# Performance work log

Hardware: AMD Instinct MI355X
Metric: run time of the kernel (lower is better)

The kernel has to match this reference:

```python
import jax, jax.numpy as jnp
import numpy as np

N_HEAD = 8
D = 512
D_K = D // N_HEAD  # 64
B, S = 8, 1024


def setup_inputs() -> dict:
    key = jax.random.key(0)
    ks = jax.random.split(key, 7)
    scale = 1.0 / np.sqrt(D)  # ~ torch Linear init range
    return {
        "q": jax.random.normal(ks[0], (B, S, D), dtype=jnp.float32),
        "k": jax.random.normal(ks[1], (B, S, D), dtype=jnp.float32),
        "v": jax.random.normal(ks[2], (B, S, D), dtype=jnp.float32),
        # per-head Q/K projection weights, torch Linear convention W:[out,in]=[d_k,d]
        "Wq": jax.random.uniform(ks[3], (N_HEAD, D_K, D), jnp.float32, -scale, scale),
        "Wk": jax.random.uniform(ks[4], (N_HEAD, D_K, D), jnp.float32, -scale, scale),
        "Wv": jax.random.uniform(ks[5], (D_K, D), jnp.float32, -scale, scale),
        "Wo": jax.random.uniform(ks[6], (D, D_K), jnpp := jnp.float32, -1.0 / np.sqrt(D_K), 1.0 / np.sqrt(D_K)),
    }


def reference(q, k, v, Wq, Wk, Wv, Wo):
    # shared V projection: [B,S,d_k]
    vs = jnp.einsum("bsd,ed->bse", v, Wv)
    # batched per-head Q/K projections: [B,H,S,d_k]
    qh = jnp.einsum("bsd,hed->bhse", q, Wq)
    kh = jnp.einsum("bsd,hed->bhse", k, Wk)
    inv_sqrt_dk = 1.0 / jnp.sqrt(jnp.asarray(D_K, q.dtype))
    # scores [B,H,Sq,Sk], softmax over keys
    scores = jnp.einsum("bhqe,bhke->bhqk", qh * inv_sqrt_dk, kh)
    attn = jax.nn.softmax(scores, axis=-1)
    # shared V across heads, then mean over heads (interpretable combine)
    heads = jnp.einsum("bhqk,bke->bhqe", attn, vs)  # [B,H,S,d_k]
    head = heads.mean(axis=1)                        # [B,S,d_k]
    out = jnp.einsum("bse,de->bsd", head, Wo)        # [B,S,d]
    # torch.stack(attention) stacks over heads first -> [H,B,Sq,Sk]
    attn_stacked = jnp.transpose(attn, (1, 0, 2, 3))
    return out, attn_stacked
```

## Files before the change

kernel.cpp:

```cpp
#include <hip/hip_runtime.h>


using short8 = __attribute__((ext_vector_type(8))) short;
using f32x4  = __attribute__((ext_vector_type(4))) float;

static __device__ __forceinline__ short f2bf(float f) {
    union { float f; unsigned u; } x; x.f = f;
    unsigned r = x.u + 0x7fffu + ((x.u >> 16) & 1u);
    return (short)(r >> 16);
}
static __device__ __forceinline__ float bfhi2f(unsigned hi_bits) {
    union { unsigned u; float f; } x; x.u = hi_bits;
    return x.f;
}

__global__ __launch_bounds__(256) void gemm_proj(
    const float* __restrict__ A, const float* __restrict__ W,
    void* __restrict__ out, int M, int N, int K, float scale, int mode)
{
    __shared__ short As[128][40];
    __shared__ short Bs[128][40];

    const int tid  = threadIdx.x;
    const int m0   = blockIdx.x * 128;
    const int n0   = blockIdx.y * 128;
    const int lane = tid & 63, wave = tid >> 6;
    const int wm   = (wave & 1) * 64, wn = (wave >> 1) * 64;
    const int lrow = lane & 15, lq = lane >> 4;

    f32x4 acc[4][4] = {};

    for (int k0 = 0; k0 < K; k0 += 32) {
#pragma unroll
        for (int i = 0; i < 4; ++i) {
            int c = tid + i * 256;
            int row = c >> 3, c4 = c & 7;
            float4 v = *(const float4*)(A + (size_t)(m0 + row) * K + k0 + c4 * 4);
            short* dst = &As[row][c4 * 4];
            dst[0] = f2bf(v.x); dst[1] = f2bf(v.y); dst[2] = f2bf(v.z); dst[3] = f2bf(v.w);
        }
#pragma unroll
        for (int i = 0; i < 4; ++i) {
            int c = tid + i * 256;
            int row = c >> 3, c4 = c & 7;
            int gn = n0 + row;
            float4 v = make_float4(0.f, 0.f, 0.f, 0.f);
            if (gn < N) v = *(const float4*)(W + (size_t)gn * K + k0 + c4 * 4);
            short* dst = &Bs[row][c4 * 4];
            dst[0] = f2bf(v.x); dst[1] = f2bf(v.y); dst[2] = f2bf(v.z); dst[3] = f2bf(v.w);
        }
        __syncthreads();

        short8 af[4], bw[4];
#pragma unroll
        for (int i = 0; i < 4; ++i)
            af[i] = *(const short8*)&As[wm + i * 16 + lrow][lq * 8];
#pragma unroll
        for (int j = 0; j < 4; ++j)
            bw[j] = *(const short8*)&Bs[wn + j * 16 + lrow][lq * 8];
#pragma unroll
        for (int i = 0; i < 4; ++i)
#pragma unroll
            for (int j = 0; j < 4; ++j)
                acc[i][j] = __builtin_amdgcn_mfma_f32_16x16x32_bf16(af[i], bw[j], acc[i][j], 0, 0, 0);
        __syncthreads();
    }

#pragma unroll
    for (int i = 0; i < 4; ++i) {
#pragma unroll
        for (int j = 0; j < 4; ++j) {
#pragma unroll
            for (int r = 0; r < 4; ++r) {
                int m = m0 + wm + i * 16 + lq * 4 + r;
                int n = n0 + wn + j * 16 + lrow;
                if (n >= N) continue;
                float val = acc[i][j][r] * scale;
                if (mode == 0) {
                    int b = m >> 10, s = m & 1023;
                    int hh = n >> 6, e = n & 63;
                    ((short*)out)[(((size_t)(b * 8 + hh) * 1024 + s) << 6) + e] = f2bf(val);
                } else if (mode == 2) {
                    int b = m >> 10, s = m & 1023;
                    ((short*)out)[(((size_t)b * 64 + n) << 10) + s] = f2bf(val);
                } else {
                    ((float*)out)[(size_t)m * N + n] = val;
                }
            }
        }
    }
}

__global__ __launch_bounds__(256) void attn_fused(
    const short* __restrict__ qh,
    const short* __restrict__ kh,
    const short* __restrict__ vt,
    float* __restrict__ attn_out,
    float* __restrict__ head)
{
    __shared__ short qs[64][72];
    __shared__ short ks[128][72];
    __shared__ short vts[64][136];
    __shared__ short pa[4][16][136];

    const int bh = blockIdx.x;
    const int b = bh >> 3, h = bh & 7;
    const int qbase = blockIdx.y << 6;
    const int tid  = threadIdx.x;
    const int lane = tid & 63, wave = tid >> 6;
    const int lrow = lane & 15, lq = lane >> 4;

    const short* qp = qh + ((size_t)bh << 16);
    const short* kp = kh + ((size_t)bh << 16);
    const short* vp = vt + ((size_t)b << 16);

#pragma unroll
    for (int i = 0; i < 2; ++i) {
        int c = tid + i * 256;
        int row = c >> 3, c8 = c & 7;
        *(uint4*)&qs[row][c8 * 8] = *(const uint4*)(qp + (size_t)(qbase + row) * 64 + c8 * 8);
    }
    __syncthreads();

    short8 qf[2];
#pragma unroll
    for (int kk = 0; kk < 2; ++kk)
        qf[kk] = *(const short8*)&qs[wave * 16 + lrow][kk * 32 + lq * 8];

    float sume[4] = {0.f, 0.f, 0.f, 0.f};
    for (int kt = 0; kt < 1024; kt += 128) {
        __syncthreads();
#pragma unroll
        for (int i = 0; i < 4; ++i) {
            int c = tid + i * 256;
            int row = c >> 3, c8 = c & 7;
            *(uint4*)&ks[row][c8 * 8] = *(const uint4*)(kp + (size_t)(kt + row) * 64 + c8 * 8);
        }
        __syncthreads();
#pragma unroll
        for (int j = 0; j < 8; ++j) {
            f32x4 sc = {0.f, 0.f, 0.f, 0.f};
            short8 kb0 = *(const short8*)&ks[j * 16 + lrow][lq * 8];
            short8 kb1 = *(const short8*)&ks[j * 16 + lrow][32 + lq * 8];
            sc = __builtin_amdgcn_mfma_f32_16x16x32_bf16(qf[0], kb0, sc, 0, 0, 0);
            sc = __builtin_amdgcn_mfma_f32_16x16x32_bf16(qf[1], kb1, sc, 0, 0, 0);
#pragma unroll
            for (int r = 0; r < 4; ++r) sume[r] += __expf(sc[r]);
        }
    }
#pragma unroll
    for (int m = 1; m <= 8; m <<= 1)
#pragma unroll
        for (int r = 0; r < 4; ++r) sume[r] += __shfl_xor(sume[r], m, 64);
    float rinv[4];
#pragma unroll
    for (int r = 0; r < 4; ++r) rinv[r] = 1.0f / sume[r];

    f32x4 hacc[4] = {};
    for (int kt = 0; kt < 1024; kt += 128) {
        __syncthreads();
#pragma unroll
        for (int i = 0; i < 4; ++i) {
            int c = tid + i * 256;
            int row = c >> 3, c8 = c & 7;
            *(uint4*)&ks[row][c8 * 8] = *(const uint4*)(kp + (size_t)(kt + row) * 64 + c8 * 8);
        }
#pragma unroll
        for (int i = 0; i < 4; ++i) {
            int c = tid + i * 256;
            int row = c >> 4, c8 = c & 15;
            *(uint4*)&vts[row][c8 * 8] = *(const uint4*)(vp + ((size_t)row << 10) + kt + c8 * 8);
        }
        __syncthreads();

#pragma unroll
        for (int j = 0; j < 8; ++j) {
            f32x4 sc = {0.f, 0.f, 0.f, 0.f};
            short8 kb0 = *(const short8*)&ks[j * 16 + lrow][lq * 8];
            short8 kb1 = *(const short8*)&ks[j * 16 + lrow][32 + lq * 8];
            sc = __builtin_amdgcn_mfma_f32_16x16x32_bf16(qf[0], kb0, sc, 0, 0, 0);
            sc = __builtin_amdgcn_mfma_f32_16x16x32_bf16(qf[1], kb1, sc, 0, 0, 0);
#pragma unroll
            for (int r = 0; r < 4; ++r)
                pa[wave][lq * 4 + r][j * 16 + lrow] = f2bf(__expf(sc[r]) * rinv[r]);
        }

        size_t abase = (((size_t)(h * 8 + b) * 1024 + qbase + wave * 16) << 10) + kt;
#pragma unroll
        for (int i = 0; i < 4; ++i) {
            int c = lane + i * 64;
            int row = c >> 4, c8 = c & 15;
            uint4 pk = *(const uint4*)&pa[wave][row][c8 * 8];
            float4 v0, v1;
            v0.x = bfhi2f(pk.x << 16); v0.y = bfhi2f(pk.x & 0xffff0000u);
            v0.z = bfhi2f(pk.y << 16); v0.w = bfhi2f(pk.y & 0xffff0000u);
            v1.x = bfhi2f(pk.z << 16); v1.y = bfhi2f(pk.z & 0xffff0000u);
            v1.z = bfhi2f(pk.w << 16); v1.w = bfhi2f(pk.w & 0xffff0000u);
            float* gdst = attn_out + abase + ((size_t)row << 10) + c8 * 8;
            *(float4*)gdst       = v0;
            *(float4*)(gdst + 4) = v1;
        }

#pragma unroll
        for (int kk = 0; kk < 4; ++kk) {
            short8 af = *(const short8*)&pa[wave][lrow][kk * 32 + lq * 8];
#pragma unroll
            for (int cc = 0; cc < 4; ++cc) {
                short8 bv = *(const short8*)&vts[cc * 16 + lrow][kk * 32 + lq * 8];
                hacc[cc] = __builtin_amdgcn_mfma_f32_16x16x32_bf16(af, bv, hacc[cc], 0, 0, 0);
            }
        }
    }

#pragma unroll
    for (int cc = 0; cc < 4; ++cc)
#pragma unroll
        for (int r = 0; r < 4; ++r) {
            float v = hacc[cc][r] * 0.125f;
            atomicAdd(&head[(((size_t)b * 1024 + qbase + wave * 16 + lq * 4 + r) << 6) + cc * 16 + lrow], v);
        }
}

extern "C" void kernel_launch(void* const* d_in, const int* in_sizes, int n_in,
                              void* d_out, int out_size, void* d_ws, size_t ws_size,
                              hipStream_t stream)
{
    (void)in_sizes; (void)n_in; (void)out_size; (void)ws_size;

    const float* q  = (const float*)d_in[0];
    const float* k  = (const float*)d_in[1];
    const float* v  = (const float*)d_in[2];
    const float* Wq = (const float*)d_in[3];
    const float* Wk = (const float*)d_in[4];
    const float* Wv = (const float*)d_in[5];
    const float* Wo = (const float*)d_in[6];

    float* out  = (float*)d_out;
    float* attn = out + (size_t)8 * 1024 * 512;

    char* ws = (char*)d_ws;
    short* qh  = (short*)(ws);
    short* kh  = (short*)(ws + ((size_t)8  << 20));
    short* vt  = (short*)(ws + ((size_t)16 << 20));
    float* head = (float*)(ws + ((size_t)17 << 20));

    hipMemsetAsync(head, 0, (size_t)8 * 1024 * 64 * sizeof(float), stream);

    gemm_proj<<<dim3(64, 4), 256, 0, stream>>>(q, Wq, qh, 8192, 512, 512, 0.125f, 0);
    gemm_proj<<<dim3(64, 4), 256, 0, stream>>>(k, Wk, kh, 8192, 512, 512, 1.0f, 0);
    gemm_proj<<<dim3(64, 1), 256, 0, stream>>>(v, Wv, vt, 8192, 64, 512, 1.0f, 2);

    attn_fused<<<dim3(64, 16), 256, 0, stream>>>(qh, kh, vt, attn, head);

    gemm_proj<<<dim3(64, 4), 256, 0, stream>>>(head, Wo, out, 8192, 512, 64, 1.0f, 3);
}
```

Before: 517.4 us.

## Split attention into score and PV kernels, materializing exp scores

Splits the fused attention kernel into a scores kernel and a PV kernel. The scores kernel computes QK^T once, stores unnormalized bf16 exponentials and row reciprocal sums to workspace. The PV kernel reads them back, writes normalized attention, and does PV. This removes the recomputation of QK^T. Head outputs are now stored per head in bf16 and reduced by a K=512 output GEMM instead of atomics plus a memset. The V-projection epilogue is transposed through LDS for coalesced stores. In exchange it adds a large intermediate write and read through global memory.

```diff
diff --git a/kernel.cpp b/kernel.cpp
--- a/kernel.cpp
+++ b/kernel.cpp
@@ -16,10 +16,12 @@
 
 __global__ __launch_bounds__(256) void gemm_proj(
     const float* __restrict__ A, const float* __restrict__ W,
-    void* __restrict__ out, int M, int N, int K, float scale, int mode)
-{
-    __shared__ short As[128][40];
-    __shared__ short Bs[128][40];
+    short* __restrict__ out, int N, int K, float scale, int mode)
+{
+    __shared__ short smem[10240];
+    short (*As)[40] = (short(*)[40])smem;
+    short (*Bs)[40] = (short(*)[40])(smem + 5120);
+    short (*ts)[136] = (short(*)[136])smem;
 
     const int tid  = threadIdx.x;
     const int m0   = blockIdx.x * 128;
@@ -66,42 +68,132 @@
         __syncthreads();
     }
 
-#pragma unroll
-    for (int i = 0; i < 4; ++i) {
-#pragma unroll
-        for (int j = 0; j < 4; ++j) {
-#pragma unroll
-            for (int r = 0; r < 4; ++r) {
-                int m = m0 + wm + i * 16 + lq * 4 + r;
-                int n = n0 + wn + j * 16 + lrow;
-                if (n >= N) continue;
-                float val = acc[i][j][r] * scale;
-                if (mode == 0) {
+    if (mode == 0) {
+#pragma unroll
+        for (int i = 0; i < 4; ++i)
+#pragma unroll
+            for (int j = 0; j < 4; ++j)
+#pragma unroll
+                for (int r = 0; r < 4; ++r) {
+                    int m = m0 + wm + i * 16 + lq * 4 + r;
+                    int n = n0 + wn + j * 16 + lrow;
                     int b = m >> 10, s = m & 1023;
                     int hh = n >> 6, e = n & 63;
-                    ((short*)out)[(((size_t)(b * 8 + hh) * 1024 + s) << 6) + e] = f2bf(val);
-                } else if (mode == 2) {
-                    int b = m >> 10, s = m & 1023;
-                    ((short*)out)[(((size_t)b * 64 + n) << 10) + s] = f2bf(val);
-                } else {
-                    ((float*)out)[(size_t)m * N + n] = val;
+                    out[(((size_t)(b * 8 + hh) * 1024 + s) << 6) + e] =
+                        f2bf(acc[i][j][r] * scale);
                 }
-            }
-        }
-    }
-}
-
-__global__ __launch_bounds__(256) void attn_fused(
-    const short* __restrict__ qh,
-    const short* __restrict__ kh,
-    const short* __restrict__ vt,
-    float* __restrict__ attn_out,
-    float* __restrict__ head)
+    } else {
+        if (wn == 0) {
+#pragma unroll
+            for (int i = 0; i < 4; ++i)
+#pragma unroll
+                for (int j = 0; j < 4; ++j)
+#pragma unroll
+                    for (int r = 0; r < 4; ++r) {
+                        int ml = wm + i * 16 + lq * 4 + r;
+                        int n  = j * 16 + lrow;
+                        ts[n][ml] = f2bf(acc[i][j][r] * scale);
+                    }
+        }
+        __syncthreads();
+        int b = m0 >> 10, s0 = m0 & 1023;
+#pragma unroll
+        for (int i = 0; i < 4; ++i) {
+            int c = tid + i * 256;
+            int row = c >> 4, c16 = c & 15;
+            *(uint4*)(out + ((size_t)(b * 64 + row) << 10) + s0 + c16 * 8) =
+                *(const uint4*)&ts[row][c16 * 8];
+        }
+    }
+}
+
+__global__ __launch_bounds__(256) void attn_scores(
+    const short* __restrict__ qh, const short* __restrict__ kh,
+    short* __restrict__ expw, float* __restrict__ rinv)
 {
     __shared__ short qs[64][72];
     __shared__ short ks[128][72];
+    __shared__ short pa[64][136];
+
+    const int bh = blockIdx.x;
+    const int qbase = blockIdx.y << 6;
+    const int tid  = threadIdx.x;
+    const int lane = tid & 63, wave = tid >> 6;
+    const int lrow = lane & 15, lq = lane >> 4;
+
+    const short* qp = qh + ((size_t)bh << 16);
+    const short* kp = kh + ((size_t)bh << 16);
+    short* ep = expw + (((size_t)(bh << 10) + qbase) << 10);
+
+#pragma unroll
+    for (int i = 0; i < 2; ++i) {
+        int c = tid + i * 256;
+        int row = c >> 3, c8 = c & 7;
+        *(uint4*)&qs[row][c8 * 8] = *(const uint4*)(qp + (size_t)(qbase + row) * 64 + c8 * 8);
+    }
+    __syncthreads();
+
+    short8 qf[2];
+#pragma unroll
+    for (int kk = 0; kk < 2; ++kk)
+        qf[kk] = *(const short8*)&qs[wave * 16 + lrow][kk * 32 + lq * 8];
+
+    float sume[4] = {0.f, 0.f, 0.f, 0.f};
+
+    for (int kt = 0; kt < 1024; kt += 128) {
+        __syncthreads();
+#pragma unroll
+        for (int i = 0; i < 4; ++i) {
+            int c = tid + i * 256;
+            int row = c >> 3, c8 = c & 7;
+            *(uint4*)&ks[row][c8 * 8] = *(const uint4*)(kp + (size_t)(kt + row) * 64 + c8 * 8);
+        }
+        __syncthreads();
+
+#pragma unroll
+        for (int j = 0; j < 8; ++j) {
+            f32x4 sc = {0.f, 0.f, 0.f, 0.f};
+            short8 kb0 = *(const short8*)&ks[j * 16 + lrow][lq * 8];
+            short8 kb1 = *(const short8*)&ks[j * 16 + lrow][32 + lq * 8];
+            sc = __builtin_amdgcn_mfma_f32_16x16x32_bf16(qf[0], kb0, sc, 0, 0, 0);
+            sc = __builtin_amdgcn_mfma_f32_16x16x32_bf16(qf[1], kb1, sc, 0, 0, 0);
+#pragma unroll
+            for (int r = 0; r < 4; ++r) {
+                float e = __expf(sc[r]);
+                sume[r] += e;
+                pa[wave * 16 + lq * 4 + r][j * 16 + lrow] = f2bf(e);
+            }
+        }
+        __syncthreads();
+
+#pragma unroll
+        for (int i = 0; i < 4; ++i) {
+            int c = tid + i * 256;
+            int row = c >> 4, c16 = c & 15;
+            *(uint4*)(ep + ((size_t)row << 10) + kt + c16 * 8) =
+                *(const uint4*)&pa[row][c16 * 8];
+        }
+    }
+
+#pragma unroll
+    for (int m = 1; m <= 8; m <<= 1)
+#pragma unroll
+        for (int r = 0; r < 4; ++r) sume[r] += __shfl_xor(sume[r], m, 64);
+    if (lrow == 0) {
+#pragma unroll
+        for (int r = 0; r < 4; ++r)
+            rinv[(bh << 10) + qbase + wave * 16 + lq * 4 + r] = 1.0f / sume[r];
+    }
+}
+
+__global__ __launch_bounds__(256) void attn_pv(
+    const short* __restrict__ expw, const float* __restrict__ rinv,
+    const short* __restrict__ vt, float* __restrict__ attn_out,
+    short* __restrict__ headbf)
+{
+    __shared__ short es[64][136];
     __shared__ short vts[64][136];
-    __shared__ short pa[4][16][136];
+    __shared__ float rs[64];
 
     const int bh = blockIdx.x;
     const int b = bh >> 3, h = bh & 7;
@@ -110,100 +202,44 @@
     const int lane = tid & 63, wave = tid >> 6;
     const int lrow = lane & 15, lq = lane >> 4;
 
-    const short* qp = qh + ((size_t)bh << 16);
-    const short* kp = kh + ((size_t)bh << 16);
+    const short* ep = expw + (((size_t)(bh << 10) + qbase) << 10);
     const short* vp = vt + ((size_t)b << 16);
 
-#pragma unroll
-    for (int i = 0; i < 2; ++i) {
-        int c = tid + i * 256;
-        int row = c >> 3, c8 = c & 7;
-        *(uint4*)&qs[row][c8 * 8] = *(const uint4*)(qp + (size_t)(qbase + row) * 64 + c8 * 8);
-    }
-    __syncthreads();
-
-    short8 qf[2];
-#pragma unroll
-    for (int kk = 0; kk < 2; ++kk)
-        qf[kk] = *(const short8*)&qs[wave * 16 + lrow][kk * 32 + lq * 8];
-
-    float sume[4] = {0.f, 0.f, 0.f, 0.f};
+    if (tid < 64) rs[tid] = rinv[(bh << 10) + qbase + tid];
+
+    f32x4 hacc[4] = {};
+    const size_t abase0 = (((size_t)(h * 8 + b) * 1024 + qbase) << 10);
+
     for (int kt = 0; kt < 1024; kt += 128) {
         __syncthreads();
 #pragma unroll
         for (int i = 0; i < 4; ++i) {
             int c = tid + i * 256;
-            int row = c >> 3, c8 = c & 7;
-            *(uint4*)&ks[row][c8 * 8] = *(const uint4*)(kp + (size_t)(kt + row) * 64 + c8 * 8);
-        }
-        __syncthreads();
-#pragma unroll
-        for (int j = 0; j < 8; ++j) {
-            f32x4 sc = {0.f, 0.f, 0.f, 0.f};
-            short8 kb0 = *(const short8*)&ks[j * 16 + lrow][lq * 8];
-            short8 kb1 = *(const short8*)&ks[j * 16 + lrow][32 + lq * 8];
-            sc = __builtin_amdgcn_mfma_f32_16x16x32_bf16(qf[0], kb0, sc, 0, 0, 0);
-            sc = __builtin_amdgcn_mfma_f32_16x16x32_bf16(qf[1], kb1, sc, 0, 0, 0);
-#pragma unroll
-            for (int r = 0; r < 4; ++r) sume[r] += __expf(sc[r]);
-        }
-    }
-#pragma unroll
-    for (int m = 1; m <= 8; m <<= 1)
-#pragma unroll
-        for (int r = 0; r < 4; ++r) sume[r] += __shfl_xor(sume[r], m, 64);
-    float rinv[4];
-#pragma unroll
-    for (int r = 0; r < 4; ++r) rinv[r] = 1.0f / sume[r];
-
-    f32x4 hacc[4] = {};
-    for (int kt = 0; kt < 1024; kt += 128) {
-        __syncthreads();
-#pragma unroll
-        for (int i = 0; i < 4; ++i) {
-            int c = tid + i * 256;
-            int row = c >> 3, c8 = c & 7;
-            *(uint4*)&ks[row][c8 * 8] = *(const uint4*)(kp + (size_t)(kt + row) * 64 + c8 * 8);
-        }
-#pragma unroll
-        for (int i = 0; i < 4; ++i) {
-            int c = tid + i * 256;
-            int row = c >> 4, c8 = c & 15;
-            *(uint4*)&vts[row][c8 * 8] = *(const uint4*)(vp + ((size_t)row << 10) + kt + c8 * 8);
-        }
-        __syncthreads();
-
-#pragma unroll
-        for (int j = 0; j < 8; ++j) {
-            f32x4 sc = {0.f, 0.f, 0.f, 0.f};
-            short8 kb0 = *(const short8*)&ks[j * 16 + lrow][lq * 8];
-            short8 kb1 = *(const short8*)&ks[j * 16 + lrow][32 + lq * 8];
-            sc = __builtin_amdgcn_mfma_f32_16x16x32_bf16(qf[0], kb0, sc, 0, 0, 0);
-            sc = __builtin_amdgcn_mfma_f32_16x16x32_bf16(qf[1], kb1, sc, 0, 0, 0);
-#pragma unroll
-            for (int r = 0; r < 4; ++r)
-                pa[wave][lq * 4 + r][j * 16 + lrow] = f2bf(__expf(sc[r]) * rinv[r]);
-        }
-
-        size_t abase = (((size_t)(h * 8 + b) * 1024 + qbase + wave * 16) << 10) + kt;
-#pragma unroll
-        for (int i = 0; i < 4; ++i) {
-            int c = lane + i * 64;
-            int row = c >> 4, c8 = c & 15;
-            uint4 pk = *(const uint4*)&pa[wave][row][c8 * 8];
+            int row = c >> 4, c16 = c & 15;
+            *(uint4*)&es[row][c16 * 8]  = *(const uint4*)(ep + ((size_t)row << 10) + kt + c16 * 8);
+            *(uint4*)&vts[row][c16 * 8] = *(const uint4*)(vp + ((size_t)row << 10) + kt + c16 * 8);
+        }
+        __syncthreads();
+
+#pragma unroll
+        for (int i = 0; i < 4; ++i) {
+            int c = tid + i * 256;
+            int row = c >> 4, c16 = c & 15;
+            float rv = rs[row];
+            uint4 pk = *(const uint4*)&es[row][c16 * 8];
             float4 v0, v1;
-            v0.x = bfhi2f(pk.x << 16); v0.y = bfhi2f(pk.x & 0xffff0000u);
-            v0.z = bfhi2f(pk.y << 16); v0.w = bfhi2f(pk.y & 0xffff0000u);
-            v1.x = bfhi2f(pk.z << 16); v1.y = bfhi2f(pk.z & 0xffff0000u);
-            v1.z = bfhi2f(pk.w << 16); v1.w = bfhi2f(pk.w & 0xffff0000u);
-            float* gdst = attn_out + abase + ((size_t)row << 10) + c8 * 8;
+            v0.x = bfhi2f(pk.x << 16) * rv; v0.y = bfhi2f(pk.x & 0xffff0000u) * rv;
+            v0.z = bfhi2f(pk.y << 16) * rv; v0.w = bfhi2f(pk.y & 0xffff0000u) * rv;
+            v1.x = bfhi2f(pk.z << 16) * rv; v1.y = bfhi2f(pk.z & 0xffff0000u) * rv;
+            v1.z = bfhi2f(pk.w << 16) * rv; v1.w = bfhi2f(pk.w & 0xffff0000u) * rv;
+            float* gdst = attn_out + abase0 + ((size_t)row << 10) + kt + c16 * 8;
             *(float4*)gdst       = v0;
             *(float4*)(gdst + 4) = v1;
         }
 
 #pragma unroll
         for (int kk = 0; kk < 4; ++kk) {
-            short8 af = *(const short8*)&pa[wave][lrow][kk * 32 + lq * 8];
+            short8 af = *(const short8*)&es[wave * 16 + lrow][kk * 32 + lq * 8];
 #pragma unroll
             for (int cc = 0; cc < 4; ++cc) {
                 short8 bv = *(const short8*)&vts[cc * 16 + lrow][kk * 32 + lq * 8];
@@ -216,9 +252,70 @@
     for (int cc = 0; cc < 4; ++cc)
 #pragma unroll
         for (int r = 0; r < 4; ++r) {
-            float v = hacc[cc][r] * 0.125f;
-            atomicAdd(&head[(((size_t)b * 1024 + qbase + wave * 16 + lq * 4 + r) << 6) + cc * 16 + lrow], v);
-        }
+            int srow = wave * 16 + lq * 4 + r;
+            float v = hacc[cc][r] * rs[srow] * 0.125f;
+            headbf[(size_t)(b * 1024 + qbase + srow) * 512 + h * 64 + cc * 16 + lrow] = f2bf(v);
+        }
+}
+
+__global__ __launch_bounds__(256) void gemm_out(
+    const short* __restrict__ A, const float* __restrict__ Wo,
+    float* __restrict__ out)
+{
+    __shared__ short As[128][40];
+    __shared__ short Bs[128][40];
+
+    const int tid  = threadIdx.x;
+    const int m0   = blockIdx.x * 128;
+    const int n0   = blockIdx.y * 128;
+    const int lane = tid & 63, wave = tid >> 6;
+    const int wm   = (wave & 1) * 64, wn = (wave >> 1) * 64;
+    const int lrow = lane & 15, lq = lane >> 4;
+
+    f32x4 acc[4][4] = {};
+
+    for (int k0 = 0; k0 < 512; k0 += 32) {
+#pragma unroll
+        for (int i = 0; i < 2; ++i) {
+            int c = tid + i * 256;
+            int row = c >> 2, c8 = c & 3;
+            *(uint4*)&As[row][c8 * 8] = *(const uint4*)(A + (size_t)(m0 + row) * 512 + k0 + c8 * 8);
+        }
+#pragma unroll
+        for (int i = 0; i < 4; ++i) {
+            int c = tid + i * 256;
+            int row = c >> 3, c4 = c & 7;
+            float4 v = *(const float4*)(Wo + (size_t)(n0 + row) * 64 + (k0 & 63) + c4 * 4);
+            short* dst = &Bs[row][c4 * 4];
+            dst[0] = f2bf(v.x); dst[1] = f2bf(v.y); dst[2] = f2bf(v.z); dst[3] = f2bf(v.w);
+        }
+        __syncthreads();
+
+        short8 af[4], bw[4];
+#pragma unroll
+        for (int i = 0; i < 4; ++i)
+            af[i] = *(const short8*)&As[wm + i * 16 + lrow][lq * 8];
+#pragma unroll
+        for (int j = 0; j < 4; ++j)
+            bw[j] = *(const short8*)&Bs[wn + j * 16 + lrow][lq * 8];
+#pragma unroll
+        for (int i = 0; i < 4; ++i)
+#pragma unroll
+            for (int j = 0; j < 4; ++j)
+                acc[i][j] = __builtin_amdgcn_mfma_f32_16x16x32_bf16(af[i], bw[j], acc[i][j], 0, 0, 0);
+        __syncthreads();
+    }
+
+#pragma unroll
+    for (int i = 0; i < 4; ++i)
+#pragma unroll
+        for (int j = 0; j < 4; ++j)
+#pragma unroll
+            for (int r = 0; r < 4; ++r) {
+                int m = m0 + wm + i * 16 + lq * 4 + r;
+                int n = n0 + wn + j * 16 + lrow;
+                out[(size_t)m * 512 + n] = acc[i][j][r];
+            }
 }
 
 extern "C" void kernel_launch(void* const* d_in, const int* in_sizes, int n_in,
@@ -239,18 +336,19 @@
     float* attn = out + (size_t)8 * 1024 * 512;
 
     char* ws = (char*)d_ws;
-    short* qh  = (short*)(ws);
-    short* kh  = (short*)(ws + ((size_t)8  << 20));
-    short* vt  = (short*)(ws + ((size_t)16 << 20));
-    float* head = (float*)(ws + ((size_t)17 << 20));
-
-    hipMemsetAsync(head, 0, (size_t)8 * 1024 * 64 * sizeof(float), stream);
-
-    gemm_proj<<<dim3(64, 4), 256, 0, stream>>>(q, Wq, qh, 8192, 512, 512, 0.125f, 0);
-    gemm_proj<<<dim3(64, 4), 256, 0, stream>>>(k, Wk, kh, 8192, 512, 512, 1.0f, 0);
-    gemm_proj<<<dim3(64, 1), 256, 0, stream>>>(v, Wv, vt, 8192, 64, 512, 1.0f, 2);
-
-    attn_fused<<<dim3(64, 16), 256, 0, stream>>>(qh, kh, vt, attn, head);
-
-    gemm_proj<<<dim3(64, 4), 256, 0, stream>>>(head, Wo, out, 8192, 512, 64, 1.0f, 3);
-}
+    short* qh     = (short*)(ws);
+    short* kh     = (short*)(ws + ((size_t)8  << 20));
+    short* vt     = (short*)(ws + ((size_t)16 << 20));
+    short* headbf = (short*)(ws + ((size_t)17 << 20));
+    float* rinvb  = (float*)(ws + ((size_t)25 << 20));
+    short* expw   = (short*)(ws + ((size_t)26 << 20));
+
+    gemm_proj<<<dim3(64, 4), 256, 0, stream>>>(q, Wq, qh, 512, 512, 0.125f, 0);
+    gemm_proj<<<dim3(64, 4), 256, 0, stream>>>(k, Wk, kh, 512, 512, 1.0f, 0);
+    gemm_proj<<<dim3(64, 1), 256, 0, stream>>>(v, Wv, vt, 64, 512, 1.0f, 2);
+
+    attn_scores<<<dim3(64, 16), 256, 0, stream>>>(qh, kh, expw, rinvb);
+    attn_pv<<<dim3(64, 16), 256, 0, stream>>>(expw, rinvb, vt, attn, headbf);
+
+    gemm_out<<<dim3(64, 4), 256, 0, stream>>>(headbf, Wo, out);
+}
```

Result: slower. 614.1 us (+18.7%).
